# Kernel optimization log

Measured on AMD Instinct MI355X. Metric: run time of the kernel, lower is better.

## Reference

```python
import jax, jax.numpy as jnp
import numpy as np
from jax import lax


def setup_inputs() -> dict:
    key = jax.random.key(0)
    k1, k2, k3 = jax.random.split(key, 3)
    B, inCh, H, Wd = 8, 64, 96, 96
    outCh, sub, kh, kw = 64, 16, 3, 3
    X = jax.random.normal(k1, (B, inCh, H, Wd), dtype=jnp.float32)
    # mimic torch Conv2d default init scale ~ 1/sqrt(fan_in)
    scale = 1.0 / np.sqrt(sub * kh * kw)
    W = jax.random.normal(k2, (outCh, sub, kh, kw), dtype=jnp.float32) * scale
    b = jax.random.normal(k3, (outCh,), dtype=jnp.float32) * scale
    return {"X": X, "W": W, "b": b}


def reference(X, W, b):
    # X: [B, inCh, H, Wd]; W: [outCh, sub, kh, kw]; b: [outCh]
    B, inCh, H, Wd = X.shape
    outCh, sub, kh, kw = W.shape
    desired = outCh + sub - 1
    reps = -(-desired // inCh)  # ceil
    # tile channels then keep first `desired` channels (matches X.repeat + slice)
    Xr = jnp.tile(X, (1, reps, 1, 1))[:, :desired]  # [B, desired, H, Wd]
    # sliding overlapping channel window: out channel o uses channels [o, o+sub)
    idx = jnp.arange(outCh)[:, None] + jnp.arange(sub)[None, :]  # [outCh, sub]
    Xw = Xr[:, idx]                         # [B, outCh, sub, H, Wd]
    Xw = Xw.reshape(B, outCh * sub, H, Wd)  # grouped-conv layout
    # grouped valid conv: group g (= out channel) contracts its own sub channels
    out = lax.conv_general_dilated(
        Xw, W, window_strides=(1, 1), padding="VALID",
        dimension_numbers=("NCHW", "OIHW", "NCHW"),
        feature_group_count=outCh,
    )  # [B, outCh, H-kh+1, Wd-kw+1]
    return out + b[None, :, None, None]
```

## Files before the change

kernel.cpp:

```cpp
#include <hip/hip_runtime.h>


typedef _Float16 f16;
typedef _Float16 f16x8 __attribute__((ext_vector_type(8)));
typedef float    f32x16 __attribute__((ext_vector_type(16)));

constexpr int IN_H = 96, IN_W = 96, OUT_H = 94, OUT_W = 94;
constexpr int NCH = 64, NOC = 64, NSUB = 16, BATCH = 8;
constexpr int NTILES = BATCH * OUT_H * 3;
constexpr size_t A_BYTES   = 2ull * 9 * 4 * 64 * 16;
constexpr size_t XN_ELEMS  = (size_t)BATCH * IN_H * IN_W * NCH;
constexpr size_t XN_OFF    = A_BYTES;
constexpr size_t WS_NEEDED = XN_OFF + XN_ELEMS * 2 + 1024;

__global__ void build_a_k(const float* __restrict__ W, f16* __restrict__ Ah)
{
    const int e = blockIdx.x * 256 + threadIdx.x;
    if (e >= 2 * 9 * 4 * 64) return;
    const int lane = e & 63;
    const int r    = e >> 6;
    const int cs   = r & 3;
    const int khw  = (r >> 2) % 9;
    const int oh   = (r >> 2) / 9;
    const int kh = khw / 3, kw = khw % 3;
    const int o  = oh * 32 + (lane & 31);
    const int cb = cs * 16 + (lane >> 5) * 8;
    f16 v[8];
#pragma unroll
    for (int j = 0; j < 8; ++j) {
        const int c = cb + j;
        const int s = (c - o) & 63;
        v[j] = (s < NSUB) ? (f16)W[((o * NSUB + s) * 3 + kh) * 3 + kw] : (f16)0.f;
    }
    *reinterpret_cast<f16x8*>(Ah + (size_t)e * 8) = *reinterpret_cast<f16x8*>(v);
}

__global__ void transpose_k(const float* __restrict__ X, f16* __restrict__ Xn)
{
    const int id = blockIdx.x;
    const int xt = id % 3;
    const int ym = id / 3;
    const int y  = ym % IN_H;
    const int b  = ym / IN_H;
    const int x  = xt * 32 + (threadIdx.x & 31);
    const int c0 = (threadIdx.x >> 5) * 8;
    const float* __restrict__ xp = X + (((size_t)(b * NCH + c0) * IN_H + y) * IN_W + x);
    f16 v[8];
#pragma unroll
    for (int i = 0; i < 8; ++i)
        v[i] = (f16)xp[(size_t)i * IN_H * IN_W];
    *reinterpret_cast<f16x8*>(Xn + ((size_t)(b * IN_H + y) * IN_W + x) * NCH + c0) =
        *reinterpret_cast<f16x8*>(v);
}

__global__ __launch_bounds__(256, 2)
void sconv_mfma(const f16* __restrict__ Ah, const f16* __restrict__ Xn,
                const float* __restrict__ Bg, float* __restrict__ Og)
{
    const int tid  = threadIdx.x;
    const int wave = tid >> 6;
    const int lane = tid & 63;
    const int oh   = wave & 1;
    const int pair = wave >> 1;
    const int px   = lane & 31;
    const int kg   = lane >> 5;

    f16x8 A[9][4];
    {
        const f16* Ab = Ah + (size_t)oh * 9 * 4 * 64 * 8;
#pragma unroll
        for (int khw = 0; khw < 9; ++khw)
#pragma unroll
            for (int cs = 0; cs < 4; ++cs)
                A[khw][cs] = *reinterpret_cast<const f16x8*>(
                    Ab + (((size_t)khw * 4 + cs) * 64 + lane) * 8);
    }
    float bv[16];
#pragma unroll
    for (int r = 0; r < 16; ++r)
        bv[r] = Bg[oh * 32 + (r & 3) + 8 * (r >> 2) + 4 * kg];

    for (int t = blockIdx.x * 2 + pair; t < NTILES; t += gridDim.x * 2) {
        const int b   = t / (OUT_H * 3);
        const int rem = t - b * (OUT_H * 3);
        const int y   = rem / 3;
        const int xg  = rem - y * 3;
        const int x0  = xg * 32;

        f32x16 acc;
#pragma unroll
        for (int r = 0; r < 16; ++r) acc[r] = 0.f;

#pragma unroll
        for (int kh = 0; kh < 3; ++kh) {
            const f16* rp = Xn + ((size_t)(b * IN_H + (y + kh)) * IN_W) * NCH;
#pragma unroll
            for (int kw = 0; kw < 3; ++kw) {
                const f16* cp = rp + (size_t)(x0 + kw + px) * NCH + kg * 8;
                f16x8 bf[4];
#pragma unroll
                for (int cs = 0; cs < 4; ++cs)
                    bf[cs] = *reinterpret_cast<const f16x8*>(cp + cs * 16);
#pragma unroll
                for (int cs = 0; cs < 4; ++cs)
                    acc = __builtin_amdgcn_mfma_f32_32x32x16_f16(
                              A[kh * 3 + kw][cs], bf[cs], acc, 0, 0, 0);
            }
        }

        const int x = x0 + px;
        if (x < OUT_W) {
#pragma unroll
            for (int r = 0; r < 16; ++r) {
                const int o = oh * 32 + (r & 3) + 8 * (r >> 2) + 4 * kg;
                Og[(((size_t)b * NOC + o) * OUT_H + y) * OUT_W + x] = acc[r] + bv[r];
            }
        }
    }
}

constexpr int TILE_X = 16, TILE_Y = 4, ROWS = TILE_Y + 2, COLS = 19;
__global__ __launch_bounds__(256, 4)
void sconv_kernel(const float* __restrict__ Xg, const float* __restrict__ Wg,
                  const float* __restrict__ Bg, float* __restrict__ Og)
{
    __shared__ float Xs[NCH][ROWS][COLS];
    const int tid = threadIdx.x, wave = tid >> 6, lane = tid & 63;
    const int x = lane & 15, y4 = lane >> 4;
    const int tx0 = blockIdx.x * TILE_X, ty0 = blockIdx.y * TILE_Y, b = blockIdx.z;
    const float* __restrict__ Xb = Xg + (size_t)b * NCH * IN_H * IN_W;
    for (int e = tid; e < NCH * ROWS * 9; e += 256) {
        const int c = e / (ROWS * 9), rm = e - c * (ROWS * 9), r = rm / 9, c2 = rm - r * 9;
        int gy = ty0 + r;      if (gy > IN_H - 1) gy = IN_H - 1;
        int gx = tx0 + 2 * c2; if (gx > IN_W - 2) gx = IN_W - 2;
        const float2 v = *reinterpret_cast<const float2*>(Xb + (c * IN_H + gy) * IN_W + gx);
        Xs[c][r][2 * c2] = v.x; Xs[c][r][2 * c2 + 1] = v.y;
    }
    __syncthreads();
    float acc[16];
#pragma unroll
    for (int i = 0; i < 16; ++i) acc[i] = 0.f;
    const int o_base = __builtin_amdgcn_readfirstlane(wave << 4);
    for (int dd = 0; dd < 31; ++dd) {
        const int c = (o_base + dd) & 63;
        float xv[3][3];
#pragma unroll
        for (int r = 0; r < 3; ++r)
#pragma unroll
            for (int kw = 0; kw < 3; ++kw) xv[r][kw] = Xs[c][y4 + r][x + kw];
#pragma unroll
        for (int jp = 0; jp < 16; ++jp)
            if ((unsigned)(dd - jp) < 16u) {
                const float* __restrict__ wp = Wg + (((o_base + jp) * NSUB) + (dd - jp)) * 9;
#pragma unroll
                for (int kh = 0; kh < 3; ++kh)
#pragma unroll
                    for (int kw = 0; kw < 3; ++kw)
                        acc[jp] = fmaf(wp[kh * 3 + kw], xv[kh][kw], acc[jp]);
            }
    }
    const int y = ty0 + y4, xo = tx0 + x;
    if (y < OUT_H && xo < OUT_W)
#pragma unroll
        for (int jp = 0; jp < 16; ++jp) {
            const int o = o_base + jp;
            Og[(((size_t)b * NOC + o) * OUT_H + y) * OUT_W + xo] = acc[jp] + Bg[o];
        }
}

extern "C" void kernel_launch(void* const* d_in, const int* in_sizes, int n_in,
                              void* d_out, int out_size, void* d_ws, size_t ws_size,
                              hipStream_t stream)
{
    const float* X = (const float*)d_in[0];
    const float* W = (const float*)d_in[1];
    const float* B = (const float*)d_in[2];
    float* O = (float*)d_out;

    if (ws_size < WS_NEEDED) {
        dim3 grid((OUT_W + TILE_X - 1) / TILE_X, (OUT_H + TILE_Y - 1) / TILE_Y, BATCH);
        sconv_kernel<<<grid, 256, 0, stream>>>(X, W, B, O);
        return;
    }

    f16* Ah = (f16*)d_ws;
    f16* Xn = (f16*)((char*)d_ws + XN_OFF);

    build_a_k<<<18, 256, 0, stream>>>(W, Ah);
    transpose_k<<<BATCH * IN_H * 3, 256, 0, stream>>>(X, Xn);
    sconv_mfma<<<512, 256, 0, stream>>>(Ah, Xn, B, O);
}
```

Measured before the change: 102.5 us.

## Skip all-zero channel blocks in MFMA conv and map one tile per wave pair

Each output-channel half only touches 3 of the 4 16-channel blocks because of the sliding 16-wide window, so the all-zero A block is dropped, leaving 27 MFMAs per tile instead of 36 and fewer B loads. The persistent grid-stride loop becomes one tile per wave pair with a launch of NTILES/2 blocks, and an XCD-aware block index remap keeps neighbouring rows on the same die. Bias is folded into the accumulator init. This trades fewer matrix instructions and loads for more block launches and per-block A-register reloads.

```diff
diff --git a/kernel.cpp b/kernel.cpp
--- a/kernel.cpp
+++ b/kernel.cpp
@@ -7,30 +7,32 @@
 
 constexpr int IN_H = 96, IN_W = 96, OUT_H = 94, OUT_W = 94;
 constexpr int NCH = 64, NOC = 64, NSUB = 16, BATCH = 8;
-constexpr int NTILES = BATCH * OUT_H * 3;
-constexpr size_t A_BYTES   = 2ull * 9 * 4 * 64 * 16;
-constexpr size_t XN_ELEMS  = (size_t)BATCH * IN_H * IN_W * NCH;
-constexpr size_t XN_OFF    = A_BYTES;
+constexpr int NSTRIP = BATCH * 3;
+constexpr int NTILES = NSTRIP * OUT_H;
+constexpr size_t A_BYTES  = 2ull * 27 * 64 * 16;
+constexpr size_t XN_ELEMS = (size_t)BATCH * IN_H * IN_W * NCH;
+constexpr size_t XN_OFF   = A_BYTES;
 constexpr size_t WS_NEEDED = XN_OFF + XN_ELEMS * 2 + 1024;
 
 __global__ void build_a_k(const float* __restrict__ W, f16* __restrict__ Ah)
 {
     const int e = blockIdx.x * 256 + threadIdx.x;
-    if (e >= 2 * 9 * 4 * 64) return;
+    if (e >= 2 * 27 * 64) return;
     const int lane = e & 63;
     const int r    = e >> 6;
-    const int cs   = r & 3;
-    const int khw  = (r >> 2) % 9;
-    const int oh   = (r >> 2) / 9;
+    const int j    = r % 3;
+    const int khw  = (r / 3) % 9;
+    const int oh   = r / 27;
+    const int cs   = oh ? (j == 0 ? 0 : j + 1) : j;
     const int kh = khw / 3, kw = khw % 3;
     const int o  = oh * 32 + (lane & 31);
     const int cb = cs * 16 + (lane >> 5) * 8;
     f16 v[8];
 #pragma unroll
-    for (int j = 0; j < 8; ++j) {
-        const int c = cb + j;
+    for (int jj = 0; jj < 8; ++jj) {
+        const int c = cb + jj;
         const int s = (c - o) & 63;
-        v[j] = (s < NSUB) ? (f16)W[((o * NSUB + s) * 3 + kh) * 3 + kw] : (f16)0.f;
+        v[jj] = (s < NSUB) ? (f16)W[((o * NSUB + s) * 3 + kh) * 3 + kw] : (f16)0.f;
     }
     *reinterpret_cast<f16x8*>(Ah + (size_t)e * 8) = *reinterpret_cast<f16x8*>(v);
 }
@@ -61,60 +63,58 @@
     const int wave = tid >> 6;
     const int lane = tid & 63;
     const int oh   = wave & 1;
-    const int pair = wave >> 1;
     const int px   = lane & 31;
     const int kg   = lane >> 5;
 
-    f16x8 A[9][4];
+    const int wg = (blockIdx.x & 7) * 141 + (blockIdx.x >> 3);
+    const int pairIdx = wg * 2 + (wave >> 1);
+    const int strip = pairIdx / OUT_H;
+    const int y     = pairIdx - strip * OUT_H;
+    const int b     = strip / 3;
+    const int xg    = strip - b * 3;
+    const int x0    = xg * 32;
+
+    f16x8 A[9][3];
     {
-        const f16* Ab = Ah + (size_t)oh * 9 * 4 * 64 * 8;
+        const f16* Ab = Ah + (size_t)oh * 27 * 64 * 8;
 #pragma unroll
         for (int khw = 0; khw < 9; ++khw)
 #pragma unroll
-            for (int cs = 0; cs < 4; ++cs)
-                A[khw][cs] = *reinterpret_cast<const f16x8*>(
-                    Ab + (((size_t)khw * 4 + cs) * 64 + lane) * 8);
+            for (int j = 0; j < 3; ++j)
+                A[khw][j] = *reinterpret_cast<const f16x8*>(
+                    Ab + (((size_t)khw * 3 + j) * 64 + lane) * 8);
     }
-    float bv[16];
+    int co[3];
+    co[0] = 0; co[1] = oh ? 32 : 16; co[2] = oh ? 48 : 32;
+
+    f32x16 acc;
 #pragma unroll
     for (int r = 0; r < 16; ++r)
-        bv[r] = Bg[oh * 32 + (r & 3) + 8 * (r >> 2) + 4 * kg];
-
-    for (int t = blockIdx.x * 2 + pair; t < NTILES; t += gridDim.x * 2) {
-        const int b   = t / (OUT_H * 3);
-        const int rem = t - b * (OUT_H * 3);
-        const int y   = rem / 3;
-        const int xg  = rem - y * 3;
-        const int x0  = xg * 32;
-
-        f32x16 acc;
-#pragma unroll
-        for (int r = 0; r < 16; ++r) acc[r] = 0.f;
+        acc[r] = Bg[oh * 32 + (r & 3) + 8 * (r >> 2) + 4 * kg];
 
 #pragma unroll
-        for (int kh = 0; kh < 3; ++kh) {
-            const f16* rp = Xn + ((size_t)(b * IN_H + (y + kh)) * IN_W) * NCH;
+    for (int kh = 0; kh < 3; ++kh) {
+        const f16* rp = Xn + ((size_t)(b * IN_H + (y + kh)) * IN_W) * NCH;
 #pragma unroll
-            for (int kw = 0; kw < 3; ++kw) {
-                const f16* cp = rp + (size_t)(x0 + kw + px) * NCH + kg * 8;
-                f16x8 bf[4];
+        for (int kw = 0; kw < 3; ++kw) {
+            const f16* cp = rp + (size_t)(x0 + kw + px) * NCH + kg * 8;
+            f16x8 bf[3];
 #pragma unroll
-                for (int cs = 0; cs < 4; ++cs)
-                    bf[cs] = *reinterpret_cast<const f16x8*>(cp + cs * 16);
+            for (int j = 0; j < 3; ++j)
+                bf[j] = *reinterpret_cast<const f16x8*>(cp + co[j]);
 #pragma unroll
-                for (int cs = 0; cs < 4; ++cs)
-                    acc = __builtin_amdgcn_mfma_f32_32x32x16_f16(
-                              A[kh * 3 + kw][cs], bf[cs], acc, 0, 0, 0);
-            }
+            for (int j = 0; j < 3; ++j)
+                acc = __builtin_amdgcn_mfma_f32_32x32x16_f16(
+                          A[kh * 3 + kw][j], bf[j], acc, 0, 0, 0);
         }
+    }
 
-        const int x = x0 + px;
-        if (x < OUT_W) {
+    const int x = x0 + px;
+    if (x < OUT_W) {
 #pragma unroll
-            for (int r = 0; r < 16; ++r) {
-                const int o = oh * 32 + (r & 3) + 8 * (r >> 2) + 4 * kg;
-                Og[(((size_t)b * NOC + o) * OUT_H + y) * OUT_W + x] = acc[r] + bv[r];
-            }
+        for (int r = 0; r < 16; ++r) {
+            const int o = oh * 32 + (r & 3) + 8 * (r >> 2) + 4 * kg;
+            Og[(((size_t)b * NOC + o) * OUT_H + y) * OUT_W + x] = acc[r];
         }
     }
 }
@@ -186,7 +186,7 @@
     f16* Ah = (f16*)d_ws;
     f16* Xn = (f16*)((char*)d_ws + XN_OFF);
 
-    build_a_k<<<18, 256, 0, stream>>>(W, Ah);
+    build_a_k<<<14, 256, 0, stream>>>(W, Ah);
     transpose_k<<<BATCH * IN_H * 3, 256, 0, stream>>>(X, Xn);
-    sconv_mfma<<<512, 256, 0, stream>>>(Ah, Xn, B, O);
+    sconv_mfma<<<NTILES / 2, 256, 0, stream>>>(Ah, Xn, B, O);
 }
```

New measurement: 100.1 us. -2.4%, faster.
